# Kernel optimization log

Hardware: AMD Instinct MI355X
Metric: run time of the kernel (lower is better)

## Reference

```python
import jax, jax.numpy as jnp
import numpy as np

B, H, W = 2, 256, 256
N = B * H * W
E = 8 * N
CIN, CMID, COUT = 32, 64, 1
EPS = 1e-5
ELU_ALPHA = 0.1


def _elu(x):
    return jnp.where(x > 0, x, ELU_ALPHA * jnp.expm1(x))


def _bn(h, g, b, m, v):
    # inference-mode batchnorm over last (channel) axis
    return (h - m) * jax.lax.rsqrt(v + EPS) * g + b


def setup_inputs() -> dict:
    key = jax.random.key(0)
    ks = jax.random.split(key, 24)
    p = lambda k, s: jax.random.normal(k, s, jnp.float32) * 0.05
    return {
        "x": jax.random.normal(ks[0], (N, CIN), jnp.float32),
        "edge_index": jax.random.randint(ks[1], (2, E), 0, N),
        "edge_weight": jax.random.uniform(ks[2], (E, 2), jnp.float32),
        "batch": jnp.repeat(jnp.arange(B, dtype=jnp.int64), H * W),
        "nrows": H,
        "ncols": W,
        # Conv2d(in, mid, 3, padding=1, bias=False)
        "conv_w": p(ks[3], (CMID, CIN, 3, 3)),
        # BatchNorm2d(mid)
        "bn2_g": jnp.ones(CMID), "bn2_b": jnp.zeros(CMID),
        "bn2_m": p(ks[4], (CMID,)), "bn2_v": jnp.abs(p(ks[5], (CMID,))) + 1.0,
        # GCNConv(mid, mid, improved=True)
        "gcn_w": p(ks[6], (CMID, CMID)), "gcn_b": p(ks[7], (CMID,)),
        # BatchNorm(mid) -- same module reused twice in the Sequential
        "bn1_g": jnp.ones(CMID), "bn1_b": jnp.zeros(CMID),
        "bn1_m": p(ks[8], (CMID,)), "bn1_v": jnp.abs(p(ks[9], (CMID,))) + 1.0,
        # TransformerConv(mid, mid, heads=1, edge_dim=2)
        "wq": p(ks[10], (CMID, CMID)), "bq": p(ks[11], (CMID,)),
        "wk": p(ks[12], (CMID, CMID)), "bk": p(ks[13], (CMID,)),
        "wv": p(ks[14], (CMID, CMID)), "bv": p(ks[15], (CMID,)),
        "we": p(ks[16], (CMID, 2)),                      # lin_edge, bias=False
        "wskip": p(ks[17], (CMID, CMID)), "bskip": p(ks[18], (CMID,)),
        # final Linear(mid, out)
        "wl": p(ks[19], (COUT, CMID)), "bl": p(ks[20], (COUT,)),
    }


def reference(x, edge_index, edge_weight, batch, nrows, ncols,
              conv_w, bn2_g, bn2_b, bn2_m, bn2_v,
              gcn_w, gcn_b, bn1_g, bn1_b, bn1_m, bn1_v,
              wq, bq, wk, bk, wv, bv, we, wskip, bskip, wl, bl):
    nbatch = B  # batch.unique().size(0)
    # GraphToConv: (N, C) -> (B, C, H, W)
    img = x.reshape(nbatch, nrows, ncols, CIN).transpose(0, 3, 1, 2)
    h = jax.lax.conv_general_dilated(img, conv_w, (1, 1), "SAME",
                                     dimension_numbers=("NCHW", "OIHW", "NCHW"))
    h = _bn(h, bn2_g[:, None, None], bn2_b[:, None, None],
            bn2_m[:, None, None], bn2_v[:, None, None])
    h = _elu(h)  # dropout2d is identity in eval
    # ConvToGraph: (B, C, H, W) -> (N, C)
    h = h.transpose(0, 2, 3, 1).reshape(N, CMID)

    # GCNConv(improved=True): A_hat = A + 2I
    row, col = edge_index[0], edge_index[1]
    ew = edge_weight[:, 1]
    si = jnp.arange(N)
    row2 = jnp.concatenate([row, si])
    col2 = jnp.concatenate([col, si])
    w2 = jnp.concatenate([ew, jnp.full((N,), 2.0, h.dtype)])
    deg = jax.ops.segment_sum(w2, col2, N)
    dinv = jnp.where(deg > 0, jax.lax.rsqrt(deg), 0.0)
    norm = dinv[row2] * w2 * dinv[col2]  # [E+N]
    hw = h @ gcn_w.T
    h = jax.ops.segment_sum(norm[:, None] * hw[row2], col2, N) + gcn_b
    h = _elu(_bn(h, bn1_g, bn1_b, bn1_m, bn1_v))

    # TransformerConv(heads=1, edge_dim=2)
    q = h @ wq.T + bq
    k = h @ wk.T + bk
    v = h @ wv.T + bv
    e = edge_weight @ we.T  # [E, CMID]
    ke = k[row] + e
    alpha = jnp.sum(q[col] * ke, axis=-1) / np.sqrt(CMID).astype(np.float32)
    amax = jax.ops.segment_max(alpha, col, N)
    amax = jnp.where(jnp.isfinite(amax), amax, 0.0)
    ex = jnp.exp(alpha - amax[col])
    denom = jax.ops.segment_sum(ex, col, N)
    attn = ex / denom[col]  # softmax over incoming edges
    msg = (v[row] + e) * attn[:, None]
    out = jax.ops.segment_sum(msg, col, N) + (h @ wskip.T + bskip)  # root_weight
    out = _bn(out, bn1_g, bn1_b, bn1_m, bn1_v)
    return out @ wl.T + bl
```

## Files before the change

### kernel.cpp

```cpp
#include <hip/hip_runtime.h>
#include <hip/hip_fp16.h>
#include <math.h>

#define CIN   32
#define CMID  64
#define HH    256
#define WW    256
#define EPSBN 1e-5f
#define ELU_A 0.1f
#define LOG2E_DIV8 0.18033688f

typedef _Float16 half8 __attribute__((ext_vector_type(8)));
typedef _Float16 half2v __attribute__((ext_vector_type(2)));
typedef float    floatx4 __attribute__((ext_vector_type(4)));

#if __has_builtin(__builtin_amdgcn_fdot2)
#define DOT2(a, b, c) __builtin_amdgcn_fdot2((a), (b), (c), false)
#else
#define DOT2(a, b, c) ((c) + (float)(a)[0] * (float)(b)[0] + (float)(a)[1] * (float)(b)[1])
#endif

__device__ __forceinline__ float elu_f(float x) {
    return x > 0.f ? x : ELU_A * (__expf(x) - 1.f);
}
__device__ __forceinline__ float wave_sum64(float v) {
#pragma unroll
    for (int off = 32; off > 0; off >>= 1) v += __shfl_xor(v, off, 64);
    return v;
}
__device__ __forceinline__ half2v shfl_xor_h2(half2v v, int off) {
    int b = __builtin_bit_cast(int, v);
    b = __shfl_xor(b, off, 64);
    return __builtin_bit_cast(half2v, b);
}

__global__ void prep_all(const float* __restrict__ cw,
                         const float* __restrict__ g2, const float* __restrict__ b2,
                         const float* __restrict__ m2, const float* __restrict__ v2,
                         const float* __restrict__ w_gcn, const float* __restrict__ w_q,
                         const float* __restrict__ w_skip, const float* __restrict__ w_k,
                         const float* __restrict__ w_v,
                         const float* __restrict__ g1, const float* __restrict__ b1,
                         const float* __restrict__ m1, const float* __restrict__ v1,
                         const float* __restrict__ wl, const float* __restrict__ bl,
                         const float* __restrict__ we,
                         __half* __restrict__ wt16, float* __restrict__ ebias,
                         __half* __restrict__ wlin, float* __restrict__ wls,
                         float* __restrict__ consts, int* __restrict__ cnt, int N) {
    int idx = blockIdx.x * 256 + threadIdx.x;
    if (idx < N) cnt[idx] = 0;
    if (idx < 5 * 2 * 4 * 64 * 8) {
        int j = idx & 7, lane = (idx >> 3) & 63, rest = idx >> 9;
        int ot = rest & 3, kt = (rest >> 2) & 1, mat = rest >> 3;
        int o = ot * 16 + (lane & 15);
        int k = kt * 32 + (lane >> 4) * 8 + j;
        const float* W = (mat == 0) ? w_gcn : (mat == 1) ? w_q :
                         (mat == 2) ? w_skip : (mat == 3) ? w_k : w_v;
        wlin[idx] = __float2half(W[o * 64 + k]);
    }
    if (idx < 36 * 64 * 8) {
        int j = idx & 7, lane = (idx >> 3) & 63, to = idx >> 9;
        int tap = to >> 2, otile = to & 3;
        int o = otile * 16 + (lane & 15);
        int k = (lane >> 4) * 8 + j;
        float s = g2[o] * rsqrtf(v2[o] + EPSBN);
        wt16[idx] = __float2half(cw[(o * 32 + k) * 9 + tap] * s);
    }
    if (idx < 64) {
        float s = g2[idx] * rsqrtf(v2[idx] + EPSBN);
        ebias[idx] = b2[idx] - m2[idx] * s;
    }
    if (blockIdx.x == 0 && threadIdx.x < 64) {
        int c = threadIdx.x;
        float s = g1[c] * rsqrtf(v1[c] + EPSBN);
        float w = wl[c] * s;
        wls[c] = w;
        float p0 = w * we[2 * c];
        float p1 = w * we[2 * c + 1];
        float p2 = wl[c] * (b1[c] - m1[c] * s);
        p0 = wave_sum64(p0);
        p1 = wave_sum64(p1);
        p2 = wave_sum64(p2);
        if (c == 0) { consts[0] = p0; consts[1] = p1; consts[2] = p2 + bl[0]; }
    }
}

__global__ __launch_bounds__(256, 2) void conv_mfma(
        const float* __restrict__ x, const __half* __restrict__ wt16,
        const float* __restrict__ ebias, const float* __restrict__ dinv,
        __half* __restrict__ h0, int ngroups) {
    const int lane = threadIdx.x & 63;
    const int wid  = (blockIdx.x * 256 + threadIdx.x) >> 6;
    const int n16 = lane & 15, quad = lane >> 4;

    half8 bf[36];
#pragma unroll
    for (int t = 0; t < 36; ++t)
        bf[t] = *reinterpret_cast<const half8*>(wt16 + ((size_t)t * 64 + lane) * 8);
    float eb[4];
#pragma unroll
    for (int ot = 0; ot < 4; ++ot) eb[ot] = ebias[ot * 16 + n16];

    for (int gidx = wid * 4; gidx < wid * 4 + 4; ++gidx) {
        if (gidx >= ngroups) return;
        const int br = gidx >> 4;
        const int c0 = (gidx & 15) << 4;
        const int r  = br & (HH - 1);
        floatx4 acc[4] = {{0.f,0.f,0.f,0.f},{0.f,0.f,0.f,0.f},
                          {0.f,0.f,0.f,0.f},{0.f,0.f,0.f,0.f}};
#pragma unroll
        for (int dr = -1; dr <= 1; ++dr) {
            int rr = r + dr;
            if (rr < 0 || rr >= HH) continue;
            const float* xrow = x + (size_t)(br + dr) * WW * CIN;
#pragma unroll
            for (int dc = -1; dc <= 1; ++dc) {
                int cc = c0 + n16 + dc;
                half8 a = {};
                if (cc >= 0 && cc < WW) {
                    const float* xp = xrow + cc * CIN + quad * 8;
                    float4 f0 = *reinterpret_cast<const float4*>(xp);
                    float4 f1 = *reinterpret_cast<const float4*>(xp + 4);
                    a[0] = (_Float16)f0.x; a[1] = (_Float16)f0.y;
                    a[2] = (_Float16)f0.z; a[3] = (_Float16)f0.w;
                    a[4] = (_Float16)f1.x; a[5] = (_Float16)f1.y;
                    a[6] = (_Float16)f1.z; a[7] = (_Float16)f1.w;
                }
                const int tap = (dr + 1) * 3 + (dc + 1);
#pragma unroll
                for (int ot = 0; ot < 4; ++ot)
                    acc[ot] = __builtin_amdgcn_mfma_f32_16x16x32_f16(a, bf[tap * 4 + ot], acc[ot], 0, 0, 0);
            }
        }
        const int nbase = br * WW + c0;
        float dv[4];
#pragma unroll
        for (int reg = 0; reg < 4; ++reg) dv[reg] = dinv[nbase + quad * 4 + reg];
        __half* hp = h0 + (size_t)nbase * 64;
#pragma unroll
        for (int ot = 0; ot < 4; ++ot) {
#pragma unroll
            for (int reg = 0; reg < 4; ++reg) {
                int px = quad * 4 + reg;
                float val = elu_f(acc[ot][reg] + eb[ot]) * dv[reg];
                hp[(size_t)px * 64 + ot * 16 + n16] = __float2half(val);
            }
        }
    }
}

__global__ void hist_kernel(const int* __restrict__ col, int* __restrict__ cnt,
                            unsigned short* __restrict__ rank, int E) {
    int e = blockIdx.x * 256 + threadIdx.x;
    if (e < E) rank[e] = (unsigned short)atomicAdd(&cnt[col[e]], 1);
}

__global__ void scan1(const int* __restrict__ cnt, int* __restrict__ bsum) {
    __shared__ int s[256];
    int t = threadIdx.x;
    int4 c = reinterpret_cast<const int4*>(cnt)[blockIdx.x * 256 + t];
    s[t] = c.x + c.y + c.z + c.w;
    __syncthreads();
    for (int off = 128; off > 0; off >>= 1) {
        if (t < off) s[t] += s[t + off];
        __syncthreads();
    }
    if (t == 0) bsum[blockIdx.x] = s[0];
}

__global__ void scan2(const int* __restrict__ bsum, int* __restrict__ boff, int nb) {
    int t = threadIdx.x;
    int b0 = (t < nb) ? bsum[t] : 0;
    int b1 = (t + 64 < nb) ? bsum[t + 64] : 0;
    int v0 = b0, v1 = b1;
#pragma unroll
    for (int off = 1; off < 64; off <<= 1) {
        int u0 = __shfl_up(v0, off, 64);
        int u1 = __shfl_up(v1, off, 64);
        if (t >= off) { v0 += u0; v1 += u1; }
    }
    int tot0 = __shfl(v0, 63, 64);
    if (t < nb) boff[t] = v0 - b0;
    if (t + 64 < nb) boff[t + 64] = tot0 + v1 - b1;
}

__global__ void scan3(const int* __restrict__ cnt, const int* __restrict__ boff,
                      int* __restrict__ rowptr, int Ntot) {
    __shared__ int lds[256];
    int t = threadIdx.x;
    int4 c = reinterpret_cast<const int4*>(cnt)[blockIdx.x * 256 + t];
    int s1 = c.x, s2 = s1 + c.y, s3 = s2 + c.z, s4 = s3 + c.w;
    lds[t] = s4;
    __syncthreads();
    for (int off = 1; off < 256; off <<= 1) {
        int v = (t >= off) ? lds[t - off] : 0;
        __syncthreads();
        lds[t] += v;
        __syncthreads();
    }
    int excl = (t > 0 ? lds[t - 1] : 0) + boff[blockIdx.x];
    int base = (blockIdx.x * 256 + t) * 4;
    rowptr[base + 0] = excl;
    rowptr[base + 1] = excl + s1;
    rowptr[base + 2] = excl + s2;
    rowptr[base + 3] = excl + s3;
    if (base + 4 == Ntot) rowptr[Ntot] = excl + s4;
}

__global__ void scatter_kernel(const int* __restrict__ ei, const float* __restrict__ ew,
                               const unsigned short* __restrict__ rank,
                               const int* __restrict__ rowptr,
                               int2* __restrict__ edges, int E) {
    int e = blockIdx.x * 256 + threadIdx.x;
    if (e >= E) return;
    int c = ei[E + e];
    int pos = rowptr[c] + (int)rank[e];
    if (pos < 0 || pos >= E) return;
    __half2 hw = __floats2half2_rn(ew[2 * e], ew[2 * e + 1]);
    int2 pk;
    pk.x = ei[e];
    pk.y = *reinterpret_cast<int*>(&hw);
    edges[pos] = pk;
}

__global__ void deg_kernel(const int* __restrict__ rowptr, const int2* __restrict__ edges,
                           float* __restrict__ dinv, int2* __restrict__ rowpair, int Ntot) {
    int n = blockIdx.x * 256 + threadIdx.x;
    if (n >= Ntot) return;
    int p0 = rowptr[n], p1 = rowptr[n + 1];
    rowpair[n] = make_int2(p0, p1);
    float s = 2.f;
    for (int p = p0; p < p1; ++p) {
        int wbits = edges[p].y;
        s += __high2float(*reinterpret_cast<__half2*>(&wbits));
    }
    dinv[n] = rsqrtf(s);
}

__global__ __launch_bounds__(256) void gcn_gather(
        const __half* __restrict__ h0s, const int2* __restrict__ edges,
        const int2* __restrict__ rowpair,
        const float* __restrict__ dinv, __half* __restrict__ agg16, int Ntot) {
    const int lane = threadIdx.x & 63;
    const int grp = lane >> 3, t = lane & 7;
    const int n = blockIdx.x * 4 + (threadIdx.x >> 6);
    if (n >= Ntot) return;
    const float din = dinv[n];
    const int2 rp = rowpair[n];
    const int p0 = rp.x, p1 = rp.y;

    half2v acc2[4] = {};
    if (grp == 0) {
        half8 hs = *reinterpret_cast<const half8*>(h0s + (size_t)n * 64 + 8 * t);
        const half2v* h2 = reinterpret_cast<const half2v*>(&hs);
        _Float16 c = (_Float16)(2.f * din);
        half2v ch = {c, c};
#pragma unroll
        for (int i = 0; i < 4; ++i) acc2[i] = ch * h2[i];
    }
    for (int p = p0; p < p1; p += 16) {
        int pe0 = p + grp, pe1 = p + 8 + grp;
        bool a0 = pe0 < p1, a1 = pe1 < p1;
        int2 e0 = edges[a0 ? pe0 : p0];
        int2 e1 = edges[a1 ? pe1 : p0];
        float w0 = __high2float(*reinterpret_cast<__half2*>(&e0.y));
        float w1 = __high2float(*reinterpret_cast<__half2*>(&e1.y));
        float c0 = a0 ? w0 * din : 0.f;
        float c1 = a1 ? w1 * din : 0.f;
        half8 hv0 = *reinterpret_cast<const half8*>(h0s + (size_t)e0.x * 64 + 8 * t);
        half8 hv1 = *reinterpret_cast<const half8*>(h0s + (size_t)e1.x * 64 + 8 * t);
        const half2v* h20 = reinterpret_cast<const half2v*>(&hv0);
        const half2v* h21 = reinterpret_cast<const half2v*>(&hv1);
        _Float16 c0h = (_Float16)c0, c1h = (_Float16)c1;
        half2v ch0 = {c0h, c0h}, ch1 = {c1h, c1h};
#pragma unroll
        for (int i = 0; i < 4; ++i) {
            acc2[i] += ch0 * h20[i];
            acc2[i] += ch1 * h21[i];
        }
    }
#pragma unroll
    for (int off = 8; off <= 32; off <<= 1)
#pragma unroll
        for (int i = 0; i < 4; ++i)
            acc2[i] += shfl_xor_h2(acc2[i], off);
    if (grp == 0) {
        half8 ov;
#pragma unroll
        for (int i = 0; i < 4; ++i) { ov[2 * i] = acc2[i][0]; ov[2 * i + 1] = acc2[i][1]; }
        *reinterpret_cast<half8*>(agg16 + (size_t)n * 64 + 8 * t) = ov;
    }
}

#define LDS_STRIDE 72
__global__ __launch_bounds__(256) void mfma_fused(
        const __half* __restrict__ in16, const __half* __restrict__ wb,
        const float* __restrict__ gcn_b, const float* __restrict__ g,
        const float* __restrict__ b, const float* __restrict__ m,
        const float* __restrict__ v,
        const float* __restrict__ bq, const float* __restrict__ bs,
        const float* __restrict__ bk, const float* __restrict__ bv,
        const float* __restrict__ wls, const float* __restrict__ we,
        __half* __restrict__ qout, __half* __restrict__ kv,
        float4* __restrict__ aux, int ngroups) {
    __shared__ _Float16 lds_h1[4][16 * LDS_STRIDE];
    const int lane = threadIdx.x & 63;
    const int n16 = lane & 15, quad = lane >> 4;
    const int wv_ = threadIdx.x >> 6;
    _Float16* myld = lds_h1[wv_];

    half8 bf1[2][4];
#pragma unroll
    for (int kt = 0; kt < 2; ++kt)
#pragma unroll
        for (int ot = 0; ot < 4; ++ot)
            bf1[kt][ot] = *reinterpret_cast<const half8*>(wb + (((size_t)kt * 4 + ot) * 64 + lane) * 8);
    half8 bf2[4][2][4];
#pragma unroll
    for (int mt = 0; mt < 4; ++mt)
#pragma unroll
        for (int kt = 0; kt < 2; ++kt)
#pragma unroll
            for (int ot = 0; ot < 4; ++ot)
                bf2[mt][kt][ot] = *reinterpret_cast<const half8*>(
                    wb + ((((size_t)(mt + 1) * 2 + kt) * 4 + ot) * 64 + lane) * 8);

    float scl[4], shf[4], bbq[4], bbs[4], bbk[4], bbv[4], wlsv[4], we0v[4], we1v[4];
#pragma unroll
    for (int ot = 0; ot < 4; ++ot) {
        int o = ot * 16 + n16;
        float s = g[o] * rsqrtf(v[o] + EPSBN);
        scl[ot] = s;
        shf[ot] = (gcn_b[o] - m[o]) * s + b[o];
        bbq[ot] = bq[o]; bbs[ot] = bs[o]; bbk[ot] = bk[o]; bbv[ot] = bv[o];
        wlsv[ot] = wls[o];
        we0v[ot] = we[2 * o]; we1v[ot] = we[2 * o + 1];
    }

    const int wid    = blockIdx.x * 4 + wv_;
    const int stride = gridDim.x * 4;
    const int trips  = (ngroups + stride - 1) / stride;
    for (int it = 0; it < trips; ++it) {
        const int gi = wid + it * stride;
        const bool active = gi < ngroups;
        const int nbase = gi * 16;
        if (active) {
            half8 a0 = *reinterpret_cast<const half8*>(in16 + (size_t)(nbase + n16) * 64 + quad * 8);
            half8 a1 = *reinterpret_cast<const half8*>(in16 + (size_t)(nbase + n16) * 64 + 32 + quad * 8);
            floatx4 acc[4] = {{0,0,0,0},{0,0,0,0},{0,0,0,0},{0,0,0,0}};
#pragma unroll
            for (int ot = 0; ot < 4; ++ot) {
                acc[ot] = __builtin_amdgcn_mfma_f32_16x16x32_f16(a0, bf1[0][ot], acc[ot], 0, 0, 0);
                acc[ot] = __builtin_amdgcn_mfma_f32_16x16x32_f16(a1, bf1[1][ot], acc[ot], 0, 0, 0);
            }
#pragma unroll
            for (int ot = 0; ot < 4; ++ot)
#pragma unroll
                for (int reg = 0; reg < 4; ++reg) {
                    float val = elu_f(acc[ot][reg] * scl[ot] + shf[ot]);
                    myld[(quad * 4 + reg) * LDS_STRIDE + ot * 16 + n16] = (_Float16)val;
                }
        }
        __syncthreads();
        if (active) {
            half8 c0 = *reinterpret_cast<const half8*>(&myld[n16 * LDS_STRIDE + quad * 8]);
            half8 c1 = *reinterpret_cast<const half8*>(&myld[n16 * LDS_STRIDE + 32 + quad * 8]);
            floatx4 aq[4] = {{0,0,0,0},{0,0,0,0},{0,0,0,0},{0,0,0,0}};
            floatx4 as[4] = {{0,0,0,0},{0,0,0,0},{0,0,0,0},{0,0,0,0}};
            floatx4 ak[4] = {{0,0,0,0},{0,0,0,0},{0,0,0,0},{0,0,0,0}};
            floatx4 av[4] = {{0,0,0,0},{0,0,0,0},{0,0,0,0},{0,0,0,0}};
#pragma unroll
            for (int ot = 0; ot < 4; ++ot) {
                aq[ot] = __builtin_amdgcn_mfma_f32_16x16x32_f16(c0, bf2[0][0][ot], aq[ot], 0, 0, 0);
                aq[ot] = __builtin_amdgcn_mfma_f32_16x16x32_f16(c1, bf2[0][1][ot], aq[ot], 0, 0, 0);
                as[ot] = __builtin_amdgcn_mfma_f32_16x16x32_f16(c0, bf2[1][0][ot], as[ot], 0, 0, 0);
                as[ot] = __builtin_amdgcn_mfma_f32_16x16x32_f16(c1, bf2[1][1][ot], as[ot], 0, 0, 0);
                ak[ot] = __builtin_amdgcn_mfma_f32_16x16x32_f16(c0, bf2[2][0][ot], ak[ot], 0, 0, 0);
                ak[ot] = __builtin_amdgcn_mfma_f32_16x16x32_f16(c1, bf2[2][1][ot], ak[ot], 0, 0, 0);
                av[ot] = __builtin_amdgcn_mfma_f32_16x16x32_f16(c0, bf2[3][0][ot], av[ot], 0, 0, 0);
                av[ot] = __builtin_amdgcn_mfma_f32_16x16x32_f16(c1, bf2[3][1][ot], av[ot], 0, 0, 0);
            }
            float psd[4] = {0,0,0,0}, pq0[4] = {0,0,0,0}, pq1[4] = {0,0,0,0};
#pragma unroll
            for (int ot = 0; ot < 4; ++ot)
#pragma unroll
                for (int reg = 0; reg < 4; ++reg) {
                    int px = nbase + quad * 4 + reg;
                    size_t off64  = (size_t)px * 64 + ot * 16 + n16;
                    size_t off128 = (size_t)px * 128 + ot * 16 + n16;
                    float qv = aq[ot][reg] + bbq[ot];
                    qout[off64]    = __float2half(qv);
                    kv[off128]     = __float2half(ak[ot][reg] + bbk[ot]);
                    kv[off128+64]  = __float2half(av[ot][reg] + bbv[ot]);
                    psd[reg] = fmaf(wlsv[ot], as[ot][reg] + bbs[ot], psd[reg]);
                    pq0[reg] = fmaf(we0v[ot], qv, pq0[reg]);
                    pq1[reg] = fmaf(we1v[ot], qv, pq1[reg]);
                }
#pragma unroll
            for (int off = 1; off <= 8; off <<= 1)
#pragma unroll
                for (int reg = 0; reg < 4; ++reg) {
                    psd[reg] += __shfl_xor(psd[reg], off, 64);
                    pq0[reg] += __shfl_xor(pq0[reg], off, 64);
                    pq1[reg] += __shfl_xor(pq1[reg], off, 64);
                }
            if (n16 == 0) {
#pragma unroll
                for (int reg = 0; reg < 4; ++reg)
                    aux[nbase + quad * 4 + reg] =
                        make_float4(pq0[reg], pq1[reg], psd[reg], 0.f);
            }
        }
        __syncthreads();
    }
}

__global__ __launch_bounds__(256) void attn_out(
        const __half* __restrict__ qh, const __half* __restrict__ kv,
        const float4* __restrict__ aux,
        const int2* __restrict__ edges, const int2* __restrict__ rowpair,
        const float* __restrict__ wls, const float* __restrict__ consts,
        float* __restrict__ out, int Ntot) {
    const int lane = threadIdx.x & 63;
    const int grp = lane >> 3, t = lane & 7;
    const int n = blockIdx.x * 4 + (threadIdx.x >> 6);
    if (n >= Ntot) return;

    half8 q8 = *reinterpret_cast<const half8*>(qh + (size_t)n * 64 + 8 * t);
    const half2v* q2 = reinterpret_cast<const half2v*>(&q8);
    float4 ax = aux[n];
    const float qe0s = ax.x * LOG2E_DIV8, qe1s = ax.y * LOG2E_DIV8;
    const int2 rp = rowpair[n];
    const int p0 = rp.x, p1 = rp.y;

    float l = 0.f, sx = 0.f, sy = 0.f;
    half2v acc2[4] = {};
    for (int p = p0; p < p1; p += 16) {
        int pe0 = p + grp, pe1 = p + 8 + grp;
        bool a0 = pe0 < p1, a1 = pe1 < p1;
        int2 e0 = edges[a0 ? pe0 : p0];
        int2 e1 = edges[a1 ? pe1 : p0];
        float2 w0 = __half22float2(*reinterpret_cast<__half2*>(&e0.y));
        float2 w1 = __half22float2(*reinterpret_cast<__half2*>(&e1.y));
        const __half* kvp0 = kv + (size_t)e0.x * 128 + 8 * t;
        const __half* kvp1 = kv + (size_t)e1.x * 128 + 8 * t;
        half8 k80 = *reinterpret_cast<const half8*>(kvp0);
        half8 v80 = *reinterpret_cast<const half8*>(kvp0 + 64);
        half8 k81 = *reinterpret_cast<const half8*>(kvp1);
        half8 v81 = *reinterpret_cast<const half8*>(kvp1 + 64);
        const half2v* k20 = reinterpret_cast<const half2v*>(&k80);
        const half2v* k21 = reinterpret_cast<const half2v*>(&k81);
        float prod0 = 0.f, prod1 = 0.f;
#pragma unroll
        for (int i = 0; i < 4; ++i) {
            prod0 = DOT2(q2[i], k20[i], prod0);
            prod1 = DOT2(q2[i], k21[i], prod1);
        }
#pragma unroll
        for (int off = 1; off <= 4; off <<= 1) {
            prod0 += __shfl_xor(prod0, off, 64);
            prod1 += __shfl_xor(prod1, off, 64);
        }
        float ex0 = a0 ? exp2f(fmaf(qe1s, w0.y, fmaf(qe0s, w0.x, prod0 * LOG2E_DIV8))) : 0.f;
        float ex1 = a1 ? exp2f(fmaf(qe1s, w1.y, fmaf(qe0s, w1.x, prod1 * LOG2E_DIV8))) : 0.f;
        l += ex0 + ex1;
        sx = fmaf(ex0, w0.x, sx); sx = fmaf(ex1, w1.x, sx);
        sy = fmaf(ex0, w0.y, sy); sy = fmaf(ex1, w1.y, sy);
        _Float16 e0h = (_Float16)ex0, e1h = (_Float16)ex1;
        half2v eh0 = {e0h, e0h}, eh1 = {e1h, e1h};
        const half2v* v20 = reinterpret_cast<const half2v*>(&v80);
        const half2v* v21 = reinterpret_cast<const half2v*>(&v81);
#pragma unroll
        for (int i = 0; i < 4; ++i) {
            acc2[i] += eh0 * v20[i];
            acc2[i] += eh1 * v21[i];
        }
    }
    float4 wlsA = reinterpret_cast<const float4*>(wls)[2 * t];
    float4 wlsB = reinterpret_cast<const float4*>(wls)[2 * t + 1];
    float pd = (float)acc2[0][0] * wlsA.x + (float)acc2[0][1] * wlsA.y
             + (float)acc2[1][0] * wlsA.z + (float)acc2[1][1] * wlsA.w
             + (float)acc2[2][0] * wlsB.x + (float)acc2[2][1] * wlsB.y
             + (float)acc2[3][0] * wlsB.z + (float)acc2[3][1] * wlsB.w;
#pragma unroll
    for (int off = 1; off <= 32; off <<= 1) pd += __shfl_xor(pd, off, 64);
#pragma unroll
    for (int off = 8; off <= 32; off <<= 1) {
        l  += __shfl_xor(l,  off, 64);
        sx += __shfl_xor(sx, off, 64);
        sy += __shfl_xor(sy, off, 64);
    }
    if (lane == 0) {
        float inv_l = (l > 0.f) ? 1.f / l : 0.f;
        out[n] = inv_l * (pd + sx * consts[0] + sy * consts[1]) + ax.z + consts[2];
    }
}

extern "C" void kernel_launch(void* const* d_in, const int* in_sizes, int n_in,
                              void* d_out, int out_size, void* d_ws, size_t ws_size,
                              hipStream_t stream) {
    const float* x      = (const float*)d_in[0];
    const int*   ei     = (const int*)d_in[1];
    const float* ew     = (const float*)d_in[2];
    const float* conv_w = (const float*)d_in[6];
    const float* bn2_g  = (const float*)d_in[7];
    const float* bn2_b  = (const float*)d_in[8];
    const float* bn2_m  = (const float*)d_in[9];
    const float* bn2_v  = (const float*)d_in[10];
    const float* gcn_w  = (const float*)d_in[11];
    const float* gcn_b  = (const float*)d_in[12];
    const float* bn1_g  = (const float*)d_in[13];
    const float* bn1_b  = (const float*)d_in[14];
    const float* bn1_m  = (const float*)d_in[15];
    const float* bn1_v  = (const float*)d_in[16];
    const float* wq     = (const float*)d_in[17];
    const float* bq     = (const float*)d_in[18];
    const float* wk     = (const float*)d_in[19];
    const float* bk     = (const float*)d_in[20];
    const float* wv     = (const float*)d_in[21];
    const float* bv     = (const float*)d_in[22];
    const float* we     = (const float*)d_in[23];
    const float* wskip  = (const float*)d_in[24];
    const float* bskip  = (const float*)d_in[25];
    const float* wl     = (const float*)d_in[26];
    const float* bl     = (const float*)d_in[27];

    const int N = in_sizes[0] / CIN;
    const int E = in_sizes[1] / 2;

    char* p = (char*)d_ws;
    auto alloc = [&](size_t bytes) {
        void* r = (void*)p;
        p += (bytes + 255) & ~(size_t)255;
        return r;
    };
    __half* wt16    = (__half*)alloc(36 * 64 * 8 * 2);
    float*  ebias   = (float*)alloc(64 * 4);
    __half* wlin    = (__half*)alloc(5 * 2 * 4 * 64 * 8 * 2);
    float*  wls     = (float*)alloc(64 * 4);
    float*  consts  = (float*)alloc(64 * 4);
    __half* bufA    = (__half*)alloc((size_t)N * 64 * 2);
    float*  bufB    = (float*)alloc((size_t)N * 64 * 4);
    __half* bufQ    = (__half*)alloc((size_t)N * 64 * 2);
    __half* agg16   = (__half*)alloc((size_t)N * 64 * 2);
    float4* aux     = (float4*)alloc((size_t)N * 16);
    float*  dinv    = (float*)alloc((size_t)N * 4);
    int*    cnt     = (int*)alloc((size_t)N * 4);
    unsigned short* rank = (unsigned short*)alloc((size_t)E * 2);
    int*    rowptr  = (int*)alloc((size_t)(N + 1) * 4);
    int2*   rowpair = (int2*)alloc((size_t)N * 8);
    int2*   edges   = (int2*)alloc((size_t)E * 8);
    int*    bsum    = (int*)alloc(256 * 4);
    int*    boff    = (int*)alloc(256 * 4);

    __half* kv = (__half*)bufB;

    prep_all<<<(N + 255) / 256, 256, 0, stream>>>(
        conv_w, bn2_g, bn2_b, bn2_m, bn2_v,
        gcn_w, wq, wskip, wk, wv,
        bn1_g, bn1_b, bn1_m, bn1_v, wl, bl, we,
        wt16, ebias, wlin, wls, consts, cnt, N);

    hist_kernel<<<(E + 255) / 256, 256, 0, stream>>>(ei + E, cnt, rank, E);
    scan1<<<N / 1024, 256, 0, stream>>>(cnt, bsum);
    scan2<<<1, 64, 0, stream>>>(bsum, boff, N / 1024);
    scan3<<<N / 1024, 256, 0, stream>>>(cnt, boff, rowptr, N);
    scatter_kernel<<<(E + 255) / 256, 256, 0, stream>>>(ei, ew, rank, rowptr, edges, E);
    deg_kernel<<<(N + 255) / 256, 256, 0, stream>>>(rowptr, edges, dinv, rowpair, N);

    const int ngroups = N / 16;
    conv_mfma<<<ngroups / 16, 256, 0, stream>>>(x, wt16, ebias, dinv, bufA, ngroups);

    gcn_gather<<<(N + 3) / 4, 256, 0, stream>>>(bufA, edges, rowpair, dinv, agg16, N);

    mfma_fused<<<512, 256, 0, stream>>>(agg16, wlin, gcn_b,
                                        bn1_g, bn1_b, bn1_m, bn1_v,
                                        bq, bskip, bk, bv, wls, we,
                                        bufQ, kv, aux, ngroups);

    attn_out<<<(N + 3) / 4, 256, 0, stream>>>(bufQ, kv, aux, edges, rowpair,
                                              wls, consts, (float*)d_out, N);
}
```

Measured before the change: 336.3 us.

## Fold degree computation into histogram/scan and use MFMA for attention dot products

Result: slower. 410.9 us (+22.2%).

```diff
diff --git a/kernel.cpp b/kernel.cpp
--- a/kernel.cpp
+++ b/kernel.cpp
@@ -46,9 +46,10 @@
                          const float* __restrict__ we,
                          __half* __restrict__ wt16, float* __restrict__ ebias,
                          __half* __restrict__ wlin, float* __restrict__ wls,
-                         float* __restrict__ consts, int* __restrict__ cnt, int N) {
+                         float* __restrict__ consts, int* __restrict__ cnt,
+                         float* __restrict__ wsum, int N) {
     int idx = blockIdx.x * 256 + threadIdx.x;
-    if (idx < N) cnt[idx] = 0;
+    if (idx < N) { cnt[idx] = 0; wsum[idx] = 0.f; }
     if (idx < 5 * 2 * 4 * 64 * 8) {
         int j = idx & 7, lane = (idx >> 3) & 63, rest = idx >> 9;
         int ot = rest & 3, kt = (rest >> 2) & 1, mat = rest >> 3;
@@ -149,10 +150,15 @@
     }
 }
 
-__global__ void hist_kernel(const int* __restrict__ col, int* __restrict__ cnt,
+__global__ void hist_kernel(const int* __restrict__ col, const float* __restrict__ ew,
+                            int* __restrict__ cnt, float* __restrict__ wsum,
                             unsigned short* __restrict__ rank, int E) {
     int e = blockIdx.x * 256 + threadIdx.x;
-    if (e < E) rank[e] = (unsigned short)atomicAdd(&cnt[col[e]], 1);
+    if (e < E) {
+        int c = col[e];
+        rank[e] = (unsigned short)atomicAdd(&cnt[c], 1);
+        atomicAdd(&wsum[c], ew[2 * e + 1]);
+    }
 }
 
 __global__ void scan1(const int* __restrict__ cnt, int* __restrict__ bsum) {
@@ -185,7 +191,9 @@
 }
 
 __global__ void scan3(const int* __restrict__ cnt, const int* __restrict__ boff,
-                      int* __restrict__ rowptr, int Ntot) {
+                      const float* __restrict__ wsum,
+                      int* __restrict__ rowptr, int2* __restrict__ rowpair,
+                      float* __restrict__ dinv, int Ntot) {
     __shared__ int lds[256];
     int t = threadIdx.x;
     int4 c = reinterpret_cast<const int4*>(cnt)[blockIdx.x * 256 + t];
@@ -205,6 +213,15 @@
     rowptr[base + 2] = excl + s2;
     rowptr[base + 3] = excl + s3;
     if (base + 4 == Ntot) rowptr[Ntot] = excl + s4;
+    rowpair[base + 0] = make_int2(excl,      excl + s1);
+    rowpair[base + 1] = make_int2(excl + s1, excl + s2);
+    rowpair[base + 2] = make_int2(excl + s2, excl + s3);
+    rowpair[base + 3] = make_int2(excl + s3, excl + s4);
+    float4 ws = reinterpret_cast<const float4*>(wsum)[blockIdx.x * 256 + t];
+    dinv[base + 0] = rsqrtf(2.f + ws.x);
+    dinv[base + 1] = rsqrtf(2.f + ws.y);
+    dinv[base + 2] = rsqrtf(2.f + ws.z);
+    dinv[base + 3] = rsqrtf(2.f + ws.w);
 }
 
 __global__ void scatter_kernel(const int* __restrict__ ei, const float* __restrict__ ew,
@@ -221,20 +238,6 @@
     pk.x = ei[e];
     pk.y = *reinterpret_cast<int*>(&hw);
     edges[pos] = pk;
-}
-
-__global__ void deg_kernel(const int* __restrict__ rowptr, const int2* __restrict__ edges,
-                           float* __restrict__ dinv, int2* __restrict__ rowpair, int Ntot) {
-    int n = blockIdx.x * 256 + threadIdx.x;
-    if (n >= Ntot) return;
-    int p0 = rowptr[n], p1 = rowptr[n + 1];
-    rowpair[n] = make_int2(p0, p1);
-    float s = 2.f;
-    for (int p = p0; p < p1; ++p) {
-        int wbits = edges[p].y;
-        s += __high2float(*reinterpret_cast<__half2*>(&wbits));
-    }
-    dinv[n] = rsqrtf(s);
 }
 
 __global__ __launch_bounds__(256) void gcn_gather(
@@ -422,77 +425,70 @@
         const float* __restrict__ wls, const float* __restrict__ consts,
         float* __restrict__ out, int Ntot) {
     const int lane = threadIdx.x & 63;
-    const int grp = lane >> 3, t = lane & 7;
+    const int n16 = lane & 15, quad = lane >> 4;
     const int n = blockIdx.x * 4 + (threadIdx.x >> 6);
     if (n >= Ntot) return;
 
-    half8 q8 = *reinterpret_cast<const half8*>(qh + (size_t)n * 64 + 8 * t);
-    const half2v* q2 = reinterpret_cast<const half2v*>(&q8);
+    half8 qa0 = *reinterpret_cast<const half8*>(qh + (size_t)n * 64 + quad * 8);
+    half8 qa1 = *reinterpret_cast<const half8*>(qh + (size_t)n * 64 + 32 + quad * 8);
     float4 ax = aux[n];
     const float qe0s = ax.x * LOG2E_DIV8, qe1s = ax.y * LOG2E_DIV8;
+    const float c0 = consts[0], c1 = consts[1], c2 = consts[2];
     const int2 rp = rowpair[n];
     const int p0 = rp.x, p1 = rp.y;
 
     float l = 0.f, sx = 0.f, sy = 0.f;
-    half2v acc2[4] = {};
+    half2v acc2[8] = {};
     for (int p = p0; p < p1; p += 16) {
-        int pe0 = p + grp, pe1 = p + 8 + grp;
-        bool a0 = pe0 < p1, a1 = pe1 < p1;
-        int2 e0 = edges[a0 ? pe0 : p0];
-        int2 e1 = edges[a1 ? pe1 : p0];
-        float2 w0 = __half22float2(*reinterpret_cast<__half2*>(&e0.y));
-        float2 w1 = __half22float2(*reinterpret_cast<__half2*>(&e1.y));
-        const __half* kvp0 = kv + (size_t)e0.x * 128 + 8 * t;
-        const __half* kvp1 = kv + (size_t)e1.x * 128 + 8 * t;
-        half8 k80 = *reinterpret_cast<const half8*>(kvp0);
-        half8 v80 = *reinterpret_cast<const half8*>(kvp0 + 64);
-        half8 k81 = *reinterpret_cast<const half8*>(kvp1);
-        half8 v81 = *reinterpret_cast<const half8*>(kvp1 + 64);
-        const half2v* k20 = reinterpret_cast<const half2v*>(&k80);
-        const half2v* k21 = reinterpret_cast<const half2v*>(&k81);
-        float prod0 = 0.f, prod1 = 0.f;
+        int pe = p + n16;
+        bool act = pe < p1;
+        int2 e = edges[act ? pe : p0];
+        float2 w = __half22float2(*reinterpret_cast<__half2*>(&e.y));
+        const __half* kp = kv + (size_t)e.x * 128 + quad * 8;
+        half8 k0 = *reinterpret_cast<const half8*>(kp);
+        half8 k1 = *reinterpret_cast<const half8*>(kp + 32);
+        half8 v0 = *reinterpret_cast<const half8*>(kp + 64);
+        half8 v1 = *reinterpret_cast<const half8*>(kp + 96);
+        floatx4 d = {0.f, 0.f, 0.f, 0.f};
+        d = __builtin_amdgcn_mfma_f32_16x16x32_f16(qa0, k0, d, 0, 0, 0);
+        d = __builtin_amdgcn_mfma_f32_16x16x32_f16(qa1, k1, d, 0, 0, 0);
+        float ex = act ? exp2f(fmaf(qe1s, w.y, fmaf(qe0s, w.x, d[0] * LOG2E_DIV8))) : 0.f;
+        l += ex;
+        sx = fmaf(ex, w.x, sx);
+        sy = fmaf(ex, w.y, sy);
+        _Float16 eh_ = (_Float16)ex;
+        half2v eh = {eh_, eh_};
+        const half2v* v20 = reinterpret_cast<const half2v*>(&v0);
+        const half2v* v21 = reinterpret_cast<const half2v*>(&v1);
 #pragma unroll
         for (int i = 0; i < 4; ++i) {
-            prod0 = DOT2(q2[i], k20[i], prod0);
-            prod1 = DOT2(q2[i], k21[i], prod1);
+            acc2[i]     += eh * v20[i];
+            acc2[4 + i] += eh * v21[i];
         }
-#pragma unroll
-        for (int off = 1; off <= 4; off <<= 1) {
-            prod0 += __shfl_xor(prod0, off, 64);
-            prod1 += __shfl_xor(prod1, off, 64);
-        }
-        float ex0 = a0 ? exp2f(fmaf(qe1s, w0.y, fmaf(qe0s, w0.x, prod0 * LOG2E_DIV8))) : 0.f;
-        float ex1 = a1 ? exp2f(fmaf(qe1s, w1.y, fmaf(qe0s, w1.x, prod1 * LOG2E_DIV8))) : 0.f;
-        l += ex0 + ex1;
-        sx = fmaf(ex0, w0.x, sx); sx = fmaf(ex1, w1.x, sx);
-        sy = fmaf(ex0, w0.y, sy); sy = fmaf(ex1, w1.y, sy);
-        _Float16 e0h = (_Float16)ex0, e1h = (_Float16)ex1;
-        half2v eh0 = {e0h, e0h}, eh1 = {e1h, e1h};
-        const half2v* v20 = reinterpret_cast<const half2v*>(&v80);
-        const half2v* v21 = reinterpret_cast<const half2v*>(&v81);
-#pragma unroll
-        for (int i = 0; i < 4; ++i) {
-            acc2[i] += eh0 * v20[i];
-            acc2[i] += eh1 * v21[i];
-        }
-    }
-    float4 wlsA = reinterpret_cast<const float4*>(wls)[2 * t];
-    float4 wlsB = reinterpret_cast<const float4*>(wls)[2 * t + 1];
-    float pd = (float)acc2[0][0] * wlsA.x + (float)acc2[0][1] * wlsA.y
-             + (float)acc2[1][0] * wlsA.z + (float)acc2[1][1] * wlsA.w
-             + (float)acc2[2][0] * wlsB.x + (float)acc2[2][1] * wlsB.y
-             + (float)acc2[3][0] * wlsB.z + (float)acc2[3][1] * wlsB.w;
+    }
+    float4 wA = *reinterpret_cast<const float4*>(wls + quad * 8);
+    float4 wB = *reinterpret_cast<const float4*>(wls + quad * 8 + 4);
+    float4 wC = *reinterpret_cast<const float4*>(wls + 32 + quad * 8);
+    float4 wD = *reinterpret_cast<const float4*>(wls + 32 + quad * 8 + 4);
+    float pd = (float)acc2[0][0] * wA.x + (float)acc2[0][1] * wA.y
+             + (float)acc2[1][0] * wA.z + (float)acc2[1][1] * wA.w
+             + (float)acc2[2][0] * wB.x + (float)acc2[2][1] * wB.y
+             + (float)acc2[3][0] * wB.z + (float)acc2[3][1] * wB.w
+             + (float)acc2[4][0] * wC.x + (float)acc2[4][1] * wC.y
+             + (float)acc2[5][0] * wC.z + (float)acc2[5][1] * wC.w
+             + (float)acc2[6][0] * wD.x + (float)acc2[6][1] * wD.y
+             + (float)acc2[7][0] * wD.z + (float)acc2[7][1] * wD.w;
+    float s = fmaf(sx, c0, sy * c1);
 #pragma unroll
     for (int off = 1; off <= 32; off <<= 1) pd += __shfl_xor(pd, off, 64);
 #pragma unroll
-    for (int off = 8; off <= 32; off <<= 1) {
-        l  += __shfl_xor(l,  off, 64);
-        sx += __shfl_xor(sx, off, 64);
-        sy += __shfl_xor(sy, off, 64);
+    for (int off = 1; off <= 8; off <<= 1) {
+        l += __shfl_xor(l, off, 64);
+        s += __shfl_xor(s, off, 64);
     }
     if (lane == 0) {
         float inv_l = (l > 0.f) ? 1.f / l : 0.f;
-        out[n] = inv_l * (pd + sx * consts[0] + sy * consts[1]) + ax.z + consts[2];
+        out[n] = inv_l * (pd + s) + ax.z + c2;
     }
 }
 
@@ -545,6 +541,7 @@
     __half* agg16   = (__half*)alloc((size_t)N * 64 * 2);
     float4* aux     = (float4*)alloc((size_t)N * 16);
     float*  dinv    = (float*)alloc((size_t)N * 4);
+    float*  wsum    = (float*)alloc((size_t)N * 4);
     int*    cnt     = (int*)alloc((size_t)N * 4);
     unsigned short* rank = (unsigned short*)alloc((size_t)E * 2);
     int*    rowptr  = (int*)alloc((size_t)(N + 1) * 4);
@@ -559,14 +556,13 @@
         conv_w, bn2_g, bn2_b, bn2_m, bn2_v,
         gcn_w, wq, wskip, wk, wv,
         bn1_g, bn1_b, bn1_m, bn1_v, wl, bl, we,
-        wt16, ebias, wlin, wls, consts, cnt, N);
-
-    hist_kernel<<<(E + 255) / 256, 256, 0, stream>>>(ei + E, cnt, rank, E);
+        wt16, ebias, wlin, wls, consts, cnt, wsum, N);
+
+    hist_kernel<<<(E + 255) / 256, 256, 0, stream>>>(ei + E, ew, cnt, wsum, rank, E);
     scan1<<<N / 1024, 256, 0, stream>>>(cnt, bsum);
     scan2<<<1, 64, 0, stream>>>(bsum, boff, N / 1024);
-    scan3<<<N / 1024, 256, 0, stream>>>(cnt, boff, rowptr, N);
+    scan3<<<N / 1024, 256, 0, stream>>>(cnt, boff, wsum, rowptr, rowpair, dinv, N);
     scatter_kernel<<<(E + 255) / 256, 256, 0, stream>>>(ei, ew, rank, rowptr, edges, E);
-    deg_kernel<<<(N + 255) / 256, 256, 0, stream>>>(rowptr, edges, dinv, rowpair, N);
 
     const int ngroups = N / 16;
     conv_mfma<<<ngroups / 16, 256, 0, stream>>>(x, wt16, ebias, dinv, bufA, ngroups);
```

## Precompute per-node V·wl dot so attention gathers a scalar instead of V rows

Applied to the files above, without the earlier changes.

New measurement: 319.7 us. 1.05x faster.

```diff
diff --git a/kernel.cpp b/kernel.cpp
--- a/kernel.cpp
+++ b/kernel.cpp
@@ -301,8 +301,8 @@
         const float* __restrict__ bq, const float* __restrict__ bs,
         const float* __restrict__ bk, const float* __restrict__ bv,
         const float* __restrict__ wls, const float* __restrict__ we,
-        __half* __restrict__ qout, __half* __restrict__ kv,
-        float4* __restrict__ aux, int ngroups) {
+        __half* __restrict__ qout, __half* __restrict__ kout,
+        float* __restrict__ vdot, float4* __restrict__ aux, int ngroups) {
     __shared__ _Float16 lds_h1[4][16 * LDS_STRIDE];
     const int lane = threadIdx.x & 63;
     const int n16 = lane & 15, quad = lane >> 4;
@@ -380,19 +380,18 @@
                 av[ot] = __builtin_amdgcn_mfma_f32_16x16x32_f16(c0, bf2[3][0][ot], av[ot], 0, 0, 0);
                 av[ot] = __builtin_amdgcn_mfma_f32_16x16x32_f16(c1, bf2[3][1][ot], av[ot], 0, 0, 0);
             }
-            float psd[4] = {0,0,0,0}, pq0[4] = {0,0,0,0}, pq1[4] = {0,0,0,0};
+            float psd[4] = {0,0,0,0}, pq0[4] = {0,0,0,0}, pq1[4] = {0,0,0,0}, pvd[4] = {0,0,0,0};
 #pragma unroll
             for (int ot = 0; ot < 4; ++ot)
 #pragma unroll
                 for (int reg = 0; reg < 4; ++reg) {
                     int px = nbase + quad * 4 + reg;
-                    size_t off64  = (size_t)px * 64 + ot * 16 + n16;
-                    size_t off128 = (size_t)px * 128 + ot * 16 + n16;
+                    size_t off64 = (size_t)px * 64 + ot * 16 + n16;
                     float qv = aq[ot][reg] + bbq[ot];
-                    qout[off64]    = __float2half(qv);
-                    kv[off128]     = __float2half(ak[ot][reg] + bbk[ot]);
-                    kv[off128+64]  = __float2half(av[ot][reg] + bbv[ot]);
+                    qout[off64] = __float2half(qv);
+                    kout[off64] = __float2half(ak[ot][reg] + bbk[ot]);
                     psd[reg] = fmaf(wlsv[ot], as[ot][reg] + bbs[ot], psd[reg]);
+                    pvd[reg] = fmaf(wlsv[ot], av[ot][reg] + bbv[ot], pvd[reg]);
                     pq0[reg] = fmaf(we0v[ot], qv, pq0[reg]);
                     pq1[reg] = fmaf(we1v[ot], qv, pq1[reg]);
                 }
@@ -401,14 +400,17 @@
 #pragma unroll
                 for (int reg = 0; reg < 4; ++reg) {
                     psd[reg] += __shfl_xor(psd[reg], off, 64);
+                    pvd[reg] += __shfl_xor(pvd[reg], off, 64);
                     pq0[reg] += __shfl_xor(pq0[reg], off, 64);
                     pq1[reg] += __shfl_xor(pq1[reg], off, 64);
                 }
             if (n16 == 0) {
 #pragma unroll
-                for (int reg = 0; reg < 4; ++reg)
+                for (int reg = 0; reg < 4; ++reg) {
                     aux[nbase + quad * 4 + reg] =
                         make_float4(pq0[reg], pq1[reg], psd[reg], 0.f);
+                    vdot[nbase + quad * 4 + reg] = pvd[reg];
+                }
             }
         }
         __syncthreads();
@@ -416,11 +418,10 @@
 }
 
 __global__ __launch_bounds__(256) void attn_out(
-        const __half* __restrict__ qh, const __half* __restrict__ kv,
-        const float4* __restrict__ aux,
+        const __half* __restrict__ qh, const __half* __restrict__ kout,
+        const float* __restrict__ vdot, const float4* __restrict__ aux,
         const int2* __restrict__ edges, const int2* __restrict__ rowpair,
-        const float* __restrict__ wls, const float* __restrict__ consts,
-        float* __restrict__ out, int Ntot) {
+        const float* __restrict__ consts, float* __restrict__ out, int Ntot) {
     const int lane = threadIdx.x & 63;
     const int grp = lane >> 3, t = lane & 7;
     const int n = blockIdx.x * 4 + (threadIdx.x >> 6);
@@ -430,11 +431,11 @@
     const half2v* q2 = reinterpret_cast<const half2v*>(&q8);
     float4 ax = aux[n];
     const float qe0s = ax.x * LOG2E_DIV8, qe1s = ax.y * LOG2E_DIV8;
+    const float c0 = consts[0], c1 = consts[1], c2 = consts[2];
     const int2 rp = rowpair[n];
     const int p0 = rp.x, p1 = rp.y;
 
-    float l = 0.f, sx = 0.f, sy = 0.f;
-    half2v acc2[4] = {};
+    float l = 0.f, sx = 0.f, sy = 0.f, pd = 0.f;
     for (int p = p0; p < p1; p += 16) {
         int pe0 = p + grp, pe1 = p + 8 + grp;
         bool a0 = pe0 < p1, a1 = pe1 < p1;
@@ -442,12 +443,10 @@
         int2 e1 = edges[a1 ? pe1 : p0];
         float2 w0 = __half22float2(*reinterpret_cast<__half2*>(&e0.y));
         float2 w1 = __half22float2(*reinterpret_cast<__half2*>(&e1.y));
-        const __half* kvp0 = kv + (size_t)e0.x * 128 + 8 * t;
-        const __half* kvp1 = kv + (size_t)e1.x * 128 + 8 * t;
-        half8 k80 = *reinterpret_cast<const half8*>(kvp0);
-        half8 v80 = *reinterpret_cast<const half8*>(kvp0 + 64);
-        half8 k81 = *reinterpret_cast<const half8*>(kvp1);
-        half8 v81 = *reinterpret_cast<const half8*>(kvp1 + 64);
+        half8 k80 = *reinterpret_cast<const half8*>(kout + (size_t)e0.x * 64 + 8 * t);
+        half8 k81 = *reinterpret_cast<const half8*>(kout + (size_t)e1.x * 64 + 8 * t);
+        float vd0 = vdot[e0.x];
+        float vd1 = vdot[e1.x];
         const half2v* k20 = reinterpret_cast<const half2v*>(&k80);
         const half2v* k21 = reinterpret_cast<const half2v*>(&k81);
         float prod0 = 0.f, prod1 = 0.f;
@@ -466,33 +465,17 @@
         l += ex0 + ex1;
         sx = fmaf(ex0, w0.x, sx); sx = fmaf(ex1, w1.x, sx);
         sy = fmaf(ex0, w0.y, sy); sy = fmaf(ex1, w1.y, sy);
-        _Float16 e0h = (_Float16)ex0, e1h = (_Float16)ex1;
-        half2v eh0 = {e0h, e0h}, eh1 = {e1h, e1h};
-        const half2v* v20 = reinterpret_cast<const half2v*>(&v80);
-        const half2v* v21 = reinterpret_cast<const half2v*>(&v81);
-#pragma unroll
-        for (int i = 0; i < 4; ++i) {
-            acc2[i] += eh0 * v20[i];
-            acc2[i] += eh1 * v21[i];
-        }
-    }
-    float4 wlsA = reinterpret_cast<const float4*>(wls)[2 * t];
-    float4 wlsB = reinterpret_cast<const float4*>(wls)[2 * t + 1];
-    float pd = (float)acc2[0][0] * wlsA.x + (float)acc2[0][1] * wlsA.y
-             + (float)acc2[1][0] * wlsA.z + (float)acc2[1][1] * wlsA.w
-             + (float)acc2[2][0] * wlsB.x + (float)acc2[2][1] * wlsB.y
-             + (float)acc2[3][0] * wlsB.z + (float)acc2[3][1] * wlsB.w;
-#pragma unroll
-    for (int off = 1; off <= 32; off <<= 1) pd += __shfl_xor(pd, off, 64);
+        pd = fmaf(ex0, vd0, pd);  pd = fmaf(ex1, vd1, pd);
+    }
+    float u = pd + fmaf(sx, c0, sy * c1);
 #pragma unroll
     for (int off = 8; off <= 32; off <<= 1) {
-        l  += __shfl_xor(l,  off, 64);
-        sx += __shfl_xor(sx, off, 64);
-        sy += __shfl_xor(sy, off, 64);
+        l += __shfl_xor(l, off, 64);
+        u += __shfl_xor(u, off, 64);
     }
     if (lane == 0) {
         float inv_l = (l > 0.f) ? 1.f / l : 0.f;
-        out[n] = inv_l * (pd + sx * consts[0] + sy * consts[1]) + ax.z + consts[2];
+        out[n] = inv_l * u + ax.z + c2;
     }
 }
 
@@ -540,9 +523,10 @@
     float*  wls     = (float*)alloc(64 * 4);
     float*  consts  = (float*)alloc(64 * 4);
     __half* bufA    = (__half*)alloc((size_t)N * 64 * 2);
-    float*  bufB    = (float*)alloc((size_t)N * 64 * 4);
+    __half* kout    = (__half*)alloc((size_t)N * 64 * 2);
     __half* bufQ    = (__half*)alloc((size_t)N * 64 * 2);
     __half* agg16   = (__half*)alloc((size_t)N * 64 * 2);
+    float*  vdot    = (float*)alloc((size_t)N * 4);
     float4* aux     = (float4*)alloc((size_t)N * 16);
     float*  dinv    = (float*)alloc((size_t)N * 4);
     int*    cnt     = (int*)alloc((size_t)N * 4);
@@ -553,8 +537,6 @@
     int*    bsum    = (int*)alloc(256 * 4);
     int*    boff    = (int*)alloc(256 * 4);
 
-    __half* kv = (__half*)bufB;
-
     prep_all<<<(N + 255) / 256, 256, 0, stream>>>(
         conv_w, bn2_g, bn2_b, bn2_m, bn2_v,
         gcn_w, wq, wskip, wk, wv,
@@ -576,8 +558,8 @@
     mfma_fused<<<512, 256, 0, stream>>>(agg16, wlin, gcn_b,
                                         bn1_g, bn1_b, bn1_m, bn1_v,
                                         bq, bskip, bk, bv, wls, we,
-                                        bufQ, kv, aux, ngroups);
-
-    attn_out<<<(N + 3) / 4, 256, 0, stream>>>(bufQ, kv, aux, edges, rowpair,
-                                              wls, consts, (float*)d_out, N);
-}
+                                        bufQ, kout, vdot, aux, ngroups);
+
+    attn_out<<<(N + 3) / 4, 256, 0, stream>>>(bufQ, kout, vdot, aux, edges, rowpair,
+                                              consts, (float*)d_out, N);
+}
```
